# Optimization experiments

Hardware: AMD Instinct MI355X
Metric: run time of the kernel (lower is better)

Reference implementation:

```python
import jax, jax.numpy as jnp
import numpy as np

N, H, HD = 512, 8, 128          # n_nodes, n_heads, h feature dim
M0, M1 = 256, 256               # mlp_units
NORM_CONST = 1.0


def setup_inputs() -> dict:
    key = jax.random.key(0)
    ks = jax.random.split(key, 16)
    def w(k, i, o, scale=1.0):
        return jax.random.normal(k, (i, o), jnp.float32) * (scale / np.sqrt(i))
    F = HD + H * H               # h_concat dim = 128 + 64 = 192
    EIN = H + 2 * F              # edge MLP input dim = 8 + 384 = 392
    return {
        "x": jax.random.normal(ks[0], (N, H, 3), jnp.float32),
        "h": jax.random.normal(ks[1], (N, HD), jnp.float32),
        # phi_e: MLP([256,256], silu, activate_final=True)
        "We0": w(ks[2], EIN, M0), "be0": jnp.zeros((M0,), jnp.float32),
        "We1": w(ks[3], M0, M1), "be1": jnp.zeros((M1,), jnp.float32),
        # phi_inf: Linear(1) + sigmoid
        "Winf": w(ks[4], M1, 1), "binf": jnp.zeros((1,), jnp.float32),
        # phi_x: MLP([256,256], silu, activate_final=True) -> Linear(n_heads) (variance-scaled small init)
        "Wx0": w(ks[5], M1, M0), "bx0": jnp.zeros((M0,), jnp.float32),
        "Wx1": w(ks[6], M0, M1), "bx1": jnp.zeros((M1,), jnp.float32),
        "Wxo": w(ks[7], M1, H, scale=0.03), "bxo": jnp.zeros((H,), jnp.float32),
        # phi_h: MLP([256,256], silu, activate_final=False)... note haiku MLP applies
        # activation between layers; final Linear(h_dim) appended in forward.
        "Wh0": w(ks[8], M1 + HD, M0), "bh0": jnp.zeros((M0,), jnp.float32),
        "Wh1": w(ks[9], M0, M1), "bh1": jnp.zeros((M1,), jnp.float32),
        "Who": w(ks[10], M1, HD), "bho": jnp.zeros((HD,), jnp.float32),
    }


def _forward(x, h, We0, be0, We1, be1, Winf, binf, Wx0, bx0, Wx1, bx1,
             Wxo, bxo, Wh0, bh0, Wh1, bh1, Who, bho):
    n, nh = x.shape[0], x.shape[1]
    silu = jax.nn.silu
    off = 1.0 - jnp.eye(n, dtype=x.dtype)                  # off-diagonal node mask
    # per-node head-pair squared distances -> [N, H*H] (diag naturally 0)
    dh = x[:, :, None, :] - x[:, None, :, :]               # [N,H,H,3]
    sqh = jnp.sum(dh * dh, axis=-1).reshape(n, nh * nh)
    hc = jnp.concatenate([h, sqh], axis=-1)                # [N, F]
    # all-pairs node diffs per head: dn[i,j,h] = x[j,h] - x[i,h]
    dn = x[None] - x[:, None]                              # [N,N,H,3]
    sqn = jnp.sum(dn * dn, axis=-1)                        # [N,N,H]
    F = hc.shape[-1]
    hc_j = jnp.broadcast_to(hc[None], (n, n, F))           # receiver-side: hc[j]
    hc_i = jnp.broadcast_to(hc[:, None], (n, n, F))        # sender-side: hc[i]
    edge_in = jnp.concatenate([sqn, hc_j, hc_i], axis=-1)  # [N,N,H+2F]
    # phi_e (activate_final=True), zero self-edges
    m = silu(silu(edge_in @ We0 + be0) @ We1 + be1) * off[:, :, None]
    # gate + message aggregation
    e = jax.nn.sigmoid(m @ Winf + binf)[..., 0] * off      # [N,N]
    m_i = jnp.einsum('ijd,ij->id', m, e)                   # [N,M1]
    # phi_x multi-head coordinate weights (tanh=False), zero self-edges
    px = (silu(silu(m @ Wx0 + bx0) @ Wx1 + bx1) @ Wxo + bxo) * off[:, :, None]
    # normalize_by_x_norm=True path
    norm = jnp.sqrt(sqn + 1e-8) + NORM_CONST               # [N,N,H]
    ndiff = (dn / norm[..., None]) * off[:, :, None, None]
    shift = jnp.einsum('ijhd,ijh->ihd', ndiff, px) / (n - 1)  # agg='mean'
    x_new = x + shift
    # phi_h with residual
    ph_in = jnp.concatenate([m_i, h], axis=-1)
    h_new = h + silu(silu(ph_in @ Wh0 + bh0) @ Wh1 + bh1) @ Who + bho
    return x_new, h_new


def reference(x, h, We0, be0, We1, be1, Winf, binf, Wx0, bx0, Wx1, bx1,
              Wxo, bxo, Wh0, bh0, Wh1, bh1, Who, bho):
    return _forward(x, h, We0, be0, We1, be1, Winf, binf, Wx0, bx0, Wx1, bx1,
                    Wxo, bxo, Wh0, bh0, Wh1, bh1, Who, bho)
```

## Files before the change

kernel.cpp:

```cpp
#include <hip/hip_runtime.h>
#include <math.h>

#define N_NODES 512
#define NH 8
#define HD 128
#define M 256
#define PITCH 264
#define JTILE 64

typedef __bf16 v8bf __attribute__((ext_vector_type(8)));
typedef float f32x4 __attribute__((ext_vector_type(4)));
typedef unsigned uint2v __attribute__((ext_vector_type(2)));

__device__ __forceinline__ float silu_f(float v) {
  return v * __builtin_amdgcn_rcpf(1.f + __expf(-v));
}
__device__ __forceinline__ float sigmoid_f(float v) {
  return __builtin_amdgcn_rcpf(1.f + __expf(-v));
}
__device__ __forceinline__ unsigned short f2bf(float f) {
  unsigned u = __float_as_uint(f);
  u += 0x7fffu + ((u >> 16) & 1u);
  return (unsigned short)(u >> 16);
}
__device__ __forceinline__ float bf2f(unsigned short s) {
  return __uint_as_float(((unsigned)s) << 16);
}
__device__ __forceinline__ unsigned cvt_pk_bf16(float lo, float hi) {
  unsigned r;
  asm("v_cvt_pk_bf16_f32 %0, %1, %2" : "=v"(r) : "v"(lo), "v"(hi));
  return r;
}

__device__ __forceinline__ void gl2lds16(const unsigned short* g, unsigned short* l) {
  __builtin_amdgcn_global_load_lds(
      (const __attribute__((address_space(1))) unsigned int*)g,
      (__attribute__((address_space(3))) unsigned int*)l, 16, 0, 0);
}

__global__ __launch_bounds__(256) void k_pre(
    const float* __restrict__ x, const float* __restrict__ h,
    const float* __restrict__ We0, const float* __restrict__ be0,
    const float* __restrict__ We1, const float* __restrict__ Wx0,
    const float* __restrict__ Wx1, const float* __restrict__ Wxo,
    unsigned short* __restrict__ wsB,
    float* __restrict__ P, float* __restrict__ Q,
    float* __restrict__ mi, float* __restrict__ shift)
{
  const int t = threadIdx.x;
  if (blockIdx.x < 816) {
    const int gid = blockIdx.x * 256 + t;
    if (gid >= 208896) return;
    float val;
    int dst;
    if (gid < 196608) {
      const int layer = gid >> 16, e = gid & 65535;
      const int k = e >> 8, n = e & 255;
      const float* W = (layer == 0) ? We1 : (layer == 1) ? Wx0 : Wx1;
      val = W[e];
      const int kt = k >> 5, w = k & 31, quad = w >> 3, j = w & 7;
      const int nt = n >> 4, lnib = n & 15;
      dst = layer * 65536 + ((kt * 16 + nt) * 64 + quad * 16 + lnib) * 8 + j;
    } else if (gid < 198656) {
      const int e = gid - 196608;
      val = Wxo[e];
      const int k = e >> 3, col = e & 7;
      const int kt = k >> 5, w = k & 31, quad = w >> 3, j = w & 7;
      dst = 196608 + (kt * 64 + quad * 16 + col) * 8 + j;
    } else if (gid < 200704) {
      const int e = gid - 198656;
      val = 0.f;
      const int k = e >> 3, col = e & 7;
      const int kt = k >> 5, w = k & 31, quad = w >> 3, j = w & 7;
      dst = 196608 + (kt * 64 + quad * 16 + col + 8) * 8 + j;
    } else if (gid < 202752) {
      const int e = gid - 200704;
      val = We0[e];
      const int j = e >> 8, n = e & 255, nt = n >> 4, lnib = n & 15;
      dst = 200704 + (nt * 64 + lnib) * 8 + j;
    } else {
      const int e = gid - 202752;
      val = 0.f;
      const int q = 1 + (e >> 11), rem = e & 2047;
      const int j = rem & 7, lnib = (rem >> 3) & 15, nt = rem >> 7;
      dst = 200704 + (nt * 64 + q * 16 + lnib) * 8 + j;
    }
    wsB[dst] = f2bf(val);
    return;
  }
  const int i = blockIdx.x - 816;
  __shared__ float s_x[24];
  __shared__ float s_hc[192];
  mi[i * M + t] = 0.f;
  if (t < 24) { shift[i * 24 + t] = 0.f; s_x[t] = x[i * 24 + t]; }
  __syncthreads();
  if (t < HD) {
    s_hc[t] = h[i * HD + t];
  } else if (t < 192) {
    const int p = t - HD, a = p >> 3, b = p & 7;
    float s = 0.f;
#pragma unroll
    for (int d = 0; d < 3; ++d) {
      const float dx = s_x[a * 3 + d] - s_x[b * 3 + d];
      s = fmaf(dx, dx, s);
    }
    s_hc[t] = s;
  }
  __syncthreads();
  float p = 0.f, q = 0.f;
  for (int k = 0; k < 192; ++k) {
    const float hv = s_hc[k];
    p = fmaf(hv, We0[(8 + k) * M + t], p);
    q = fmaf(hv, We0[(200 + k) * M + t], q);
  }
  P[i * M + t] = p;
  Q[i * M + t] = q + be0[t];
}

__global__ __launch_bounds__(256, 2) void k_edge(
    const float* __restrict__ x,
    const float* __restrict__ P, const float* __restrict__ Q,
    const float* __restrict__ be1,
    const float* __restrict__ Winf, const float* __restrict__ binf,
    const float* __restrict__ bx0, const float* __restrict__ bx1,
    const float* __restrict__ bxo,
    const unsigned short* __restrict__ wsB,
    float* __restrict__ mi_acc, float* __restrict__ shift_acc)
{
  const int i  = blockIdx.x;
  const int j0 = blockIdx.y * JTILE;
  const int t  = threadIdx.x;
  const int lane = t & 63, wq = t >> 6;
  const int lnib = lane & 15, quad = lane >> 4;
  const int cb = wq * 64;

  __shared__ __align__(16) unsigned short a_act[JTILE * PITCH];
  __shared__ __align__(16) unsigned short B_buf[2][8192];
  __shared__ __align__(16) float s_sqn[JTILE][8];
  __shared__ __align__(16) unsigned short s_sqnb[JTILE][8];
  __shared__ float s_red[JTILE][4];
  __shared__ float s_e[JTILE];

  auto stage = [&](const unsigned short* __restrict__ Bg, int kt, int which) {
    const unsigned short* src = Bg + kt * 8192 + wq * 2048 + lane * 8;
    unsigned short* dst = &B_buf[which][wq * 2048];
    gl2lds16(src,        dst);
    gl2lds16(src + 512,  dst + 512);
    gl2lds16(src + 1024, dst + 1024);
    gl2lds16(src + 1536, dst + 1536);
  };

#pragma unroll
  for (int kk = 0; kk < 2; ++kk) {
    const int idx = kk * 256 + t;
    const int r = idx >> 3, hh = idx & 7;
    const int j = j0 + r;
    float s = 0.f;
#pragma unroll
    for (int d = 0; d < 3; ++d) {
      const float dx = x[j * 24 + hh * 3 + d] - x[i * 24 + hh * 3 + d];
      s = fmaf(dx, dx, s);
    }
    s_sqn[r][hh] = s;
    s_sqnb[r][hh] = f2bf(s);
  }

  stage(wsB, 0, 0);
  const float binf0 = binf[0];
  __syncthreads();

  f32x4 acc[4][4];

  {
#pragma unroll
    for (int ct = 0; ct < 4; ++ct)
#pragma unroll
      for (int et = 0; et < 4; ++et)
        acc[ct][et] = *(const f32x4*)&P[(j0 + et * 16 + lnib) * M + cb + ct * 16 + quad * 4];
    const unsigned short* W0 = wsB + 200704;
    v8bf wf[4], af[4];
#pragma unroll
    for (int ct = 0; ct < 4; ++ct)
      wf[ct] = *(const v8bf*)&W0[((wq * 4 + ct) * 64 + lane) * 8];
#pragma unroll
    for (int et = 0; et < 4; ++et)
      af[et] = *(const v8bf*)&s_sqnb[et * 16 + lnib][0];
#pragma unroll
    for (int ct = 0; ct < 4; ++ct)
#pragma unroll
      for (int et = 0; et < 4; ++et)
        acc[ct][et] = __builtin_amdgcn_mfma_f32_16x16x32_bf16(wf[ct], af[et], acc[ct][et], 0, 0, 0);
#pragma unroll
    for (int ct = 0; ct < 4; ++ct) {
      const f32x4 qv = *(const f32x4*)&Q[i * M + cb + ct * 16 + quad * 4];
#pragma unroll
      for (int et = 0; et < 4; ++et) {
        const int row = et * 16 + lnib;
        const unsigned w0 = cvt_pk_bf16(silu_f(acc[ct][et][0] + qv[0]),
                                        silu_f(acc[ct][et][1] + qv[1]));
        const unsigned w1 = cvt_pk_bf16(silu_f(acc[ct][et][2] + qv[2]),
                                        silu_f(acc[ct][et][3] + qv[3]));
        *(uint2v*)&a_act[row * PITCH + cb + ct * 16 + quad * 4] = (uint2v){w0, w1};
      }
    }
  }

  auto run_gemm = [&](const unsigned short* __restrict__ Bg,
                      const unsigned short* __restrict__ Bnext) {
    __syncthreads();
#pragma unroll
    for (int kt = 0; kt < 8; ++kt) {
      if (kt < 7)      stage(Bg, kt + 1, (kt + 1) & 1);
      else if (Bnext)  stage(Bnext, 0, 0);
      v8bf wf[4], af[4];
#pragma unroll
      for (int ct = 0; ct < 4; ++ct)
        wf[ct] = *(const v8bf*)&B_buf[kt & 1][(wq * 4 + ct) * 512 + lane * 8];
#pragma unroll
      for (int et = 0; et < 4; ++et)
        af[et] = *(const v8bf*)&a_act[(et * 16 + lnib) * PITCH + kt * 32 + quad * 8];
#pragma unroll
      for (int ct = 0; ct < 4; ++ct)
#pragma unroll
        for (int et = 0; et < 4; ++et)
          acc[ct][et] = __builtin_amdgcn_mfma_f32_16x16x32_bf16(wf[ct], af[et], acc[ct][et], 0, 0, 0);
      __syncthreads();
    }
  };

#pragma unroll
  for (int ct = 0; ct < 4; ++ct) {
    const f32x4 b = *(const f32x4*)&be1[cb + ct * 16 + quad * 4];
#pragma unroll
    for (int et = 0; et < 4; ++et) acc[ct][et] = b;
  }
  run_gemm(wsB, wsB + 65536);
  {
    float ge[4] = {0.f, 0.f, 0.f, 0.f};
#pragma unroll
    for (int ct = 0; ct < 4; ++ct) {
      const f32x4 wv = *(const f32x4*)&Winf[cb + ct * 16 + quad * 4];
#pragma unroll
      for (int et = 0; et < 4; ++et) {
        const int row = et * 16 + lnib;
        const bool dz = (j0 + row == i);
        const float v0 = dz ? 0.f : silu_f(acc[ct][et][0]);
        const float v1 = dz ? 0.f : silu_f(acc[ct][et][1]);
        const float v2 = dz ? 0.f : silu_f(acc[ct][et][2]);
        const float v3 = dz ? 0.f : silu_f(acc[ct][et][3]);
        ge[et] = fmaf(v0, wv[0], ge[et]);
        ge[et] = fmaf(v1, wv[1], ge[et]);
        ge[et] = fmaf(v2, wv[2], ge[et]);
        ge[et] = fmaf(v3, wv[3], ge[et]);
        *(uint2v*)&a_act[row * PITCH + cb + ct * 16 + quad * 4] =
            (uint2v){cvt_pk_bf16(v0, v1), cvt_pk_bf16(v2, v3)};
      }
    }
#pragma unroll
    for (int et = 0; et < 4; ++et) {
      float g = ge[et];
      g += __shfl_xor(g, 16);
      g += __shfl_xor(g, 32);
      if (quad == 0) s_red[et * 16 + lnib][wq] = g;
    }
  }
  __syncthreads();
  if (t < JTILE)
    s_e[t] = sigmoid_f(s_red[t][0] + s_red[t][1] + s_red[t][2] + s_red[t][3] + binf0);
  __syncthreads();

  {
    const int r0 = wq * 16;
    float m0 = 0.f, m1 = 0.f, m2 = 0.f, m3 = 0.f;
#pragma unroll
    for (int r = 0; r < 16; ++r) {
      const float ev = s_e[r0 + r];
      const unsigned pa = *(const unsigned*)&a_act[(r0 + r) * PITCH + lane * 2];
      const unsigned pb = *(const unsigned*)&a_act[(r0 + r) * PITCH + 128 + lane * 2];
      m0 = fmaf(bf2f((unsigned short)(pa & 0xffffu)), ev, m0);
      m1 = fmaf(bf2f((unsigned short)(pa >> 16)), ev, m1);
      m2 = fmaf(bf2f((unsigned short)(pb & 0xffffu)), ev, m2);
      m3 = fmaf(bf2f((unsigned short)(pb >> 16)), ev, m3);
    }
    atomicAdd(&mi_acc[i * M + lane * 2 + 0], m0);
    atomicAdd(&mi_acc[i * M + lane * 2 + 1], m1);
    atomicAdd(&mi_acc[i * M + 128 + lane * 2 + 0], m2);
    atomicAdd(&mi_acc[i * M + 128 + lane * 2 + 1], m3);
  }

#pragma unroll
  for (int ct = 0; ct < 4; ++ct) {
    const f32x4 b = *(const f32x4*)&bx0[cb + ct * 16 + quad * 4];
#pragma unroll
    for (int et = 0; et < 4; ++et) acc[ct][et] = b;
  }
  run_gemm(wsB + 65536, wsB + 131072);
#pragma unroll
  for (int ct = 0; ct < 4; ++ct)
#pragma unroll
    for (int et = 0; et < 4; ++et) {
      const int row = et * 16 + lnib;
      const unsigned w0 = cvt_pk_bf16(silu_f(acc[ct][et][0]), silu_f(acc[ct][et][1]));
      const unsigned w1 = cvt_pk_bf16(silu_f(acc[ct][et][2]), silu_f(acc[ct][et][3]));
      *(uint2v*)&a_act[row * PITCH + cb + ct * 16 + quad * 4] = (uint2v){w0, w1};
    }

#pragma unroll
  for (int ct = 0; ct < 4; ++ct) {
    const f32x4 b = *(const f32x4*)&bx1[cb + ct * 16 + quad * 4];
#pragma unroll
    for (int et = 0; et < 4; ++et) acc[ct][et] = b;
  }
  run_gemm(wsB + 131072, nullptr);
#pragma unroll
  for (int ct = 0; ct < 4; ++ct)
#pragma unroll
    for (int et = 0; et < 4; ++et) {
      const int row = et * 16 + lnib;
      const unsigned w0 = cvt_pk_bf16(silu_f(acc[ct][et][0]), silu_f(acc[ct][et][1]));
      const unsigned w1 = cvt_pk_bf16(silu_f(acc[ct][et][2]), silu_f(acc[ct][et][3]));
      *(uint2v*)&a_act[row * PITCH + cb + ct * 16 + quad * 4] = (uint2v){w0, w1};
    }
  __syncthreads();

  {
    const int e0 = wq * 16;
    f32x4 px;
    if (quad < 2) px = *(const f32x4*)&bxo[quad * 4];
    else          px = (f32x4){0.f, 0.f, 0.f, 0.f};
    const unsigned short* Bx = wsB + 196608;
#pragma unroll
    for (int kt = 0; kt < 8; ++kt) {
      const v8bf af = *(const v8bf*)&a_act[(e0 + lnib) * PITCH + kt * 32 + quad * 8];
      const v8bf wf = *(const v8bf*)&Bx[(kt * 64 + lane) * 8];
      px = __builtin_amdgcn_mfma_f32_16x16x32_bf16(wf, af, px, 0, 0, 0);
    }
    const int jg = j0 + e0 + lnib;
    float c0[4], c1[4], c2[4];
#pragma unroll
    for (int r = 0; r < 4; ++r) { c0[r] = 0.f; c1[r] = 0.f; c2[r] = 0.f; }
    if (quad < 2 && jg != i) {
#pragma unroll
      for (int r = 0; r < 4; ++r) {
        const int hh = quad * 4 + r;
        const float sq = s_sqn[e0 + lnib][hh];
        const float f  = px[r] * __builtin_amdgcn_rcpf(sqrtf(sq + 1e-8f) + 1.f);
        c0[r] = (x[jg * 24 + hh * 3 + 0] - x[i * 24 + hh * 3 + 0]) * f;
        c1[r] = (x[jg * 24 + hh * 3 + 1] - x[i * 24 + hh * 3 + 1]) * f;
        c2[r] = (x[jg * 24 + hh * 3 + 2] - x[i * 24 + hh * 3 + 2]) * f;
      }
    }
#pragma unroll
    for (int r = 0; r < 4; ++r) {
#pragma unroll
      for (int s = 1; s <= 8; s <<= 1) {
        c0[r] += __shfl_xor(c0[r], s);
        c1[r] += __shfl_xor(c1[r], s);
        c2[r] += __shfl_xor(c2[r], s);
      }
    }
    if (lnib == 0 && quad < 2) {
#pragma unroll
      for (int r = 0; r < 4; ++r) {
        const int hh = quad * 4 + r;
        atomicAdd(&shift_acc[i * 24 + hh * 3 + 0], c0[r]);
        atomicAdd(&shift_acc[i * 24 + hh * 3 + 1], c1[r]);
        atomicAdd(&shift_acc[i * 24 + hh * 3 + 2], c2[r]);
      }
    }
  }
}

__global__ __launch_bounds__(256) void k_hout(
    const float* __restrict__ x, const float* __restrict__ shift,
    const float* __restrict__ h, const float* __restrict__ mi,
    const float* __restrict__ Wh0, const float* __restrict__ bh0,
    const float* __restrict__ Wh1, const float* __restrict__ bh1,
    const float* __restrict__ Who, const float* __restrict__ bho,
    float* __restrict__ out_x, float* __restrict__ out_h)
{
  const int i = blockIdx.x, t = threadIdx.x;
  __shared__ float s_in[M + HD];
  __shared__ float s_b[M];
  if (t < 24) out_x[i * 24 + t] = x[i * 24 + t] + shift[i * 24 + t] * (1.f / 511.f);
  s_in[t] = mi[i * M + t];
  if (t < HD) s_in[M + t] = h[i * HD + t];
  __syncthreads();
  float acc = bh0[t];
  for (int k = 0; k < M + HD; ++k) acc = fmaf(s_in[k], Wh0[k * M + t], acc);
  s_b[t] = silu_f(acc);
  __syncthreads();
  float acc2 = bh1[t];
  for (int k = 0; k < M; ++k) acc2 = fmaf(s_b[k], Wh1[k * M + t], acc2);
  const float a1v = silu_f(acc2);
  __syncthreads();
  s_in[t] = a1v;
  __syncthreads();
  if (t < HD) {
    float o = bho[t];
    for (int k = 0; k < M; ++k) o = fmaf(s_in[k], Who[k * HD + t], o);
    out_h[i * HD + t] = h[i * HD + t] + o;
  }
}

extern "C" void kernel_launch(void* const* d_in, const int* in_sizes, int n_in,
                              void* d_out, int out_size, void* d_ws, size_t ws_size,
                              hipStream_t stream)
{
  const float* x    = (const float*)d_in[0];
  const float* h    = (const float*)d_in[1];
  const float* We0  = (const float*)d_in[2];
  const float* be0  = (const float*)d_in[3];
  const float* We1  = (const float*)d_in[4];
  const float* be1  = (const float*)d_in[5];
  const float* Winf = (const float*)d_in[6];
  const float* binf = (const float*)d_in[7];
  const float* Wx0  = (const float*)d_in[8];
  const float* bx0  = (const float*)d_in[9];
  const float* Wx1  = (const float*)d_in[10];
  const float* bx1  = (const float*)d_in[11];
  const float* Wxo  = (const float*)d_in[12];
  const float* bxo  = (const float*)d_in[13];
  const float* Wh0  = (const float*)d_in[14];
  const float* bh0  = (const float*)d_in[15];
  const float* Wh1  = (const float*)d_in[16];
  const float* bh1  = (const float*)d_in[17];
  const float* Who  = (const float*)d_in[18];
  const float* bho  = (const float*)d_in[19];

  float* out_x = (float*)d_out;
  float* out_h = out_x + N_NODES * NH * 3;

  float* ws    = (float*)d_ws;
  float* mi    = ws;
  float* shift = ws + 131072;
  float* P     = ws + 143360;
  float* Q     = ws + 274432;
  unsigned short* wsB = (unsigned short*)(ws + 405504);

  k_pre<<<816 + N_NODES, 256, 0, stream>>>(
      x, h, We0, be0, We1, Wx0, Wx1, Wxo, wsB, P, Q, mi, shift);
  k_edge<<<dim3(N_NODES, N_NODES / JTILE), 256, 0, stream>>>(
      x, P, Q, be1, Winf, binf, bx0, bx1, bxo, wsB, mi, shift);
  k_hout<<<N_NODES, 256, 0, stream>>>(
      x, shift, h, mi, Wh0, bh0, Wh1, bh1, Who, bho, out_x, out_h);
}
```

Measured before the change: 332.4 us.

## Read weights directly from global, fragment-major LDS activations, register-based message reduction

Removes the LDS double-buffered weight staging and has each wave load MFMA weight fragments straight from global memory (L2-resident). Activations are stored in LDS in a fragment-major layout so each MFMA operand is one contiguous 16-byte read per lane, which removes the padded pitch. The gated message sum m_i is now computed from values kept in registers, reduced with shuffles, and followed by fewer atomics. The smaller LDS footprint allows launch bounds of 3 blocks per SM. The cost is global-load latency inside the GEMM loop with no prefetch to hide it, and extra barriers around each GEMM.

```diff
diff --git a/kernel.cpp b/kernel.cpp
--- a/kernel.cpp
+++ b/kernel.cpp
@@ -5,7 +5,6 @@
 #define NH 8
 #define HD 128
 #define M 256
-#define PITCH 264
 #define JTILE 64
 
 typedef __bf16 v8bf __attribute__((ext_vector_type(8)));
@@ -23,19 +22,16 @@
   u += 0x7fffu + ((u >> 16) & 1u);
   return (unsigned short)(u >> 16);
 }
-__device__ __forceinline__ float bf2f(unsigned short s) {
-  return __uint_as_float(((unsigned)s) << 16);
+__device__ __forceinline__ float bf2f_lo(unsigned u) {
+  return __uint_as_float(u << 16);
+}
+__device__ __forceinline__ float bf2f_hi(unsigned u) {
+  return __uint_as_float(u & 0xffff0000u);
 }
 __device__ __forceinline__ unsigned cvt_pk_bf16(float lo, float hi) {
   unsigned r;
   asm("v_cvt_pk_bf16_f32 %0, %1, %2" : "=v"(r) : "v"(lo), "v"(hi));
   return r;
-}
-
-__device__ __forceinline__ void gl2lds16(const unsigned short* g, unsigned short* l) {
-  __builtin_amdgcn_global_load_lds(
-      (const __attribute__((address_space(1))) unsigned int*)g,
-      (__attribute__((address_space(3))) unsigned int*)l, 16, 0, 0);
 }
 
 __global__ __launch_bounds__(256) void k_pre(
@@ -117,7 +113,7 @@
   Q[i * M + t] = q + be0[t];
 }
 
-__global__ __launch_bounds__(256, 2) void k_edge(
+__global__ __launch_bounds__(256, 3) void k_edge(
     const float* __restrict__ x,
     const float* __restrict__ P, const float* __restrict__ Q,
     const float* __restrict__ be1,
@@ -134,20 +130,37 @@
   const int lnib = lane & 15, quad = lane >> 4;
   const int cb = wq * 64;
 
-  __shared__ __align__(16) unsigned short a_act[JTILE * PITCH];
-  __shared__ __align__(16) unsigned short B_buf[2][8192];
+  __shared__ __align__(16) unsigned short a_act[32 * 512];
   __shared__ __align__(16) float s_sqn[JTILE][8];
   __shared__ __align__(16) unsigned short s_sqnb[JTILE][8];
   __shared__ float s_red[JTILE][4];
   __shared__ float s_e[JTILE];
 
-  auto stage = [&](const unsigned short* __restrict__ Bg, int kt, int which) {
-    const unsigned short* src = Bg + kt * 8192 + wq * 2048 + lane * 8;
-    unsigned short* dst = &B_buf[which][wq * 2048];
-    gl2lds16(src,        dst);
-    gl2lds16(src + 512,  dst + 512);
-    gl2lds16(src + 1024, dst + 1024);
-    gl2lds16(src + 1536, dst + 1536);
+  f32x4 acc[4][4];
+
+  auto store_frag = [&](int ct, int et, unsigned w0, unsigned w1) {
+    const int tile = et * 8 + 2 * wq + (ct >> 1);
+    const int qp   = (ct & 1) * 2 + (quad >> 1);
+    const int sidx = (tile * 64 + qp * 16 + lnib) * 8 + (quad & 1) * 4;
+    *(uint2v*)&a_act[sidx] = (uint2v){w0, w1};
+  };
+
+  auto run_gemm = [&](const unsigned short* __restrict__ Bg) {
+#pragma unroll
+    for (int kt = 0; kt < 8; ++kt) {
+      v8bf wf[4], af[4];
+#pragma unroll
+      for (int ct = 0; ct < 4; ++ct)
+        wf[ct] = *(const v8bf*)&Bg[((kt * 16 + wq * 4 + ct) * 64 + lane) * 8];
+#pragma unroll
+      for (int et = 0; et < 4; ++et)
+        af[et] = *(const v8bf*)&a_act[((et * 8 + kt) * 64 + lane) * 8];
+#pragma unroll
+      for (int ct = 0; ct < 4; ++ct)
+#pragma unroll
+        for (int et = 0; et < 4; ++et)
+          acc[ct][et] = __builtin_amdgcn_mfma_f32_16x16x32_bf16(wf[ct], af[et], acc[ct][et], 0, 0, 0);
+    }
   };
 
 #pragma unroll
@@ -164,12 +177,8 @@
     s_sqn[r][hh] = s;
     s_sqnb[r][hh] = f2bf(s);
   }
-
-  stage(wsB, 0, 0);
   const float binf0 = binf[0];
   __syncthreads();
-
-  f32x4 acc[4][4];
 
   {
 #pragma unroll
@@ -195,38 +204,14 @@
       const f32x4 qv = *(const f32x4*)&Q[i * M + cb + ct * 16 + quad * 4];
 #pragma unroll
       for (int et = 0; et < 4; ++et) {
-        const int row = et * 16 + lnib;
         const unsigned w0 = cvt_pk_bf16(silu_f(acc[ct][et][0] + qv[0]),
                                         silu_f(acc[ct][et][1] + qv[1]));
         const unsigned w1 = cvt_pk_bf16(silu_f(acc[ct][et][2] + qv[2]),
                                         silu_f(acc[ct][et][3] + qv[3]));
-        *(uint2v*)&a_act[row * PITCH + cb + ct * 16 + quad * 4] = (uint2v){w0, w1};
-      }
-    }
-  }
-
-  auto run_gemm = [&](const unsigned short* __restrict__ Bg,
-                      const unsigned short* __restrict__ Bnext) {
-    __syncthreads();
-#pragma unroll
-    for (int kt = 0; kt < 8; ++kt) {
-      if (kt < 7)      stage(Bg, kt + 1, (kt + 1) & 1);
-      else if (Bnext)  stage(Bnext, 0, 0);
-      v8bf wf[4], af[4];
-#pragma unroll
-      for (int ct = 0; ct < 4; ++ct)
-        wf[ct] = *(const v8bf*)&B_buf[kt & 1][(wq * 4 + ct) * 512 + lane * 8];
-#pragma unroll
-      for (int et = 0; et < 4; ++et)
-        af[et] = *(const v8bf*)&a_act[(et * 16 + lnib) * PITCH + kt * 32 + quad * 8];
-#pragma unroll
-      for (int ct = 0; ct < 4; ++ct)
-#pragma unroll
-        for (int et = 0; et < 4; ++et)
-          acc[ct][et] = __builtin_amdgcn_mfma_f32_16x16x32_bf16(wf[ct], af[et], acc[ct][et], 0, 0, 0);
-      __syncthreads();
-    }
-  };
+        store_frag(ct, et, w0, w1);
+      }
+    }
+  }
 
 #pragma unroll
   for (int ct = 0; ct < 4; ++ct) {
@@ -234,7 +219,11 @@
 #pragma unroll
     for (int et = 0; et < 4; ++et) acc[ct][et] = b;
   }
-  run_gemm(wsB, wsB + 65536);
+  __syncthreads();
+  run_gemm(wsB);
+  __syncthreads();
+
+  unsigned mw[4][4][2];
   {
     float ge[4] = {0.f, 0.f, 0.f, 0.f};
 #pragma unroll
@@ -252,8 +241,10 @@
         ge[et] = fmaf(v1, wv[1], ge[et]);
         ge[et] = fmaf(v2, wv[2], ge[et]);
         ge[et] = fmaf(v3, wv[3], ge[et]);
-        *(uint2v*)&a_act[row * PITCH + cb + ct * 16 + quad * 4] =
-            (uint2v){cvt_pk_bf16(v0, v1), cvt_pk_bf16(v2, v3)};
+        const unsigned w0 = cvt_pk_bf16(v0, v1);
+        const unsigned w1 = cvt_pk_bf16(v2, v3);
+        mw[ct][et][0] = w0; mw[ct][et][1] = w1;
+        store_frag(ct, et, w0, w1);
       }
     }
 #pragma unroll
@@ -270,22 +261,39 @@
   __syncthreads();
 
   {
-    const int r0 = wq * 16;
-    float m0 = 0.f, m1 = 0.f, m2 = 0.f, m3 = 0.f;
-#pragma unroll
-    for (int r = 0; r < 16; ++r) {
-      const float ev = s_e[r0 + r];
-      const unsigned pa = *(const unsigned*)&a_act[(r0 + r) * PITCH + lane * 2];
-      const unsigned pb = *(const unsigned*)&a_act[(r0 + r) * PITCH + 128 + lane * 2];
-      m0 = fmaf(bf2f((unsigned short)(pa & 0xffffu)), ev, m0);
-      m1 = fmaf(bf2f((unsigned short)(pa >> 16)), ev, m1);
-      m2 = fmaf(bf2f((unsigned short)(pb & 0xffffu)), ev, m2);
-      m3 = fmaf(bf2f((unsigned short)(pb >> 16)), ev, m3);
-    }
-    atomicAdd(&mi_acc[i * M + lane * 2 + 0], m0);
-    atomicAdd(&mi_acc[i * M + lane * 2 + 1], m1);
-    atomicAdd(&mi_acc[i * M + 128 + lane * 2 + 0], m2);
-    atomicAdd(&mi_acc[i * M + 128 + lane * 2 + 1], m3);
+    float ev[4];
+#pragma unroll
+    for (int et = 0; et < 4; ++et) ev[et] = s_e[et * 16 + lnib];
+    float s[4][4];
+#pragma unroll
+    for (int ct = 0; ct < 4; ++ct) {
+      s[ct][0] = 0.f; s[ct][1] = 0.f; s[ct][2] = 0.f; s[ct][3] = 0.f;
+#pragma unroll
+      for (int et = 0; et < 4; ++et) {
+        s[ct][0] = fmaf(bf2f_lo(mw[ct][et][0]), ev[et], s[ct][0]);
+        s[ct][1] = fmaf(bf2f_hi(mw[ct][et][0]), ev[et], s[ct][1]);
+        s[ct][2] = fmaf(bf2f_lo(mw[ct][et][1]), ev[et], s[ct][2]);
+        s[ct][3] = fmaf(bf2f_hi(mw[ct][et][1]), ev[et], s[ct][3]);
+      }
+    }
+#pragma unroll
+    for (int ct = 0; ct < 4; ++ct)
+#pragma unroll
+      for (int r = 0; r < 4; ++r) {
+        float v = s[ct][r];
+        v += __shfl_xor(v, 1);
+        v += __shfl_xor(v, 2);
+        v += __shfl_xor(v, 4);
+        v += __shfl_xor(v, 8);
+        s[ct][r] = v;
+      }
+    if (lnib == 0) {
+#pragma unroll
+      for (int ct = 0; ct < 4; ++ct)
+#pragma unroll
+        for (int r = 0; r < 4; ++r)
+          atomicAdd(&mi_acc[i * M + cb + ct * 16 + quad * 4 + r], s[ct][r]);
+    }
   }
 
 #pragma unroll
@@ -294,15 +302,15 @@
 #pragma unroll
     for (int et = 0; et < 4; ++et) acc[ct][et] = b;
   }
-  run_gemm(wsB + 65536, wsB + 131072);
+  run_gemm(wsB + 65536);
+  __syncthreads();
 #pragma unroll
   for (int ct = 0; ct < 4; ++ct)
 #pragma unroll
     for (int et = 0; et < 4; ++et) {
-      const int row = et * 16 + lnib;
       const unsigned w0 = cvt_pk_bf16(silu_f(acc[ct][et][0]), silu_f(acc[ct][et][1]));
       const unsigned w1 = cvt_pk_bf16(silu_f(acc[ct][et][2]), silu_f(acc[ct][et][3]));
-      *(uint2v*)&a_act[row * PITCH + cb + ct * 16 + quad * 4] = (uint2v){w0, w1};
+      store_frag(ct, et, w0, w1);
     }
 
 #pragma unroll
@@ -311,30 +319,31 @@
 #pragma unroll
     for (int et = 0; et < 4; ++et) acc[ct][et] = b;
   }
-  run_gemm(wsB + 131072, nullptr);
+  __syncthreads();
+  run_gemm(wsB + 131072);
+  __syncthreads();
 #pragma unroll
   for (int ct = 0; ct < 4; ++ct)
 #pragma unroll
     for (int et = 0; et < 4; ++et) {
-      const int row = et * 16 + lnib;
       const unsigned w0 = cvt_pk_bf16(silu_f(acc[ct][et][0]), silu_f(acc[ct][et][1]));
       const unsigned w1 = cvt_pk_bf16(silu_f(acc[ct][et][2]), silu_f(acc[ct][et][3]));
-      *(uint2v*)&a_act[row * PITCH + cb + ct * 16 + quad * 4] = (uint2v){w0, w1};
+      store_frag(ct, et, w0, w1);
     }
   __syncthreads();
 
   {
-    const int e0 = wq * 16;
     f32x4 px;
     if (quad < 2) px = *(const f32x4*)&bxo[quad * 4];
     else          px = (f32x4){0.f, 0.f, 0.f, 0.f};
     const unsigned short* Bx = wsB + 196608;
 #pragma unroll
     for (int kt = 0; kt < 8; ++kt) {
-      const v8bf af = *(const v8bf*)&a_act[(e0 + lnib) * PITCH + kt * 32 + quad * 8];
+      const v8bf af = *(const v8bf*)&a_act[((wq * 8 + kt) * 64 + lane) * 8];
       const v8bf wf = *(const v8bf*)&Bx[(kt * 64 + lane) * 8];
       px = __builtin_amdgcn_mfma_f32_16x16x32_bf16(wf, af, px, 0, 0, 0);
     }
+    const int e0 = wq * 16;
     const int jg = j0 + e0 + lnib;
     float c0[4], c1[4], c2[4];
 #pragma unroll
```

After: 285.0 us. 14.3% less time.
